# Performance work log

Measured on AMD Instinct MI355X. Metric: run time of the kernel, lower is better.

Reference implementation:

```python
import jax, jax.numpy as jnp
import numpy as np

SIZE = 416
STRIDES = (8, 16, 32)
A = 3            # anchors per scale
C = 20           # num classes
CONF_THRESH = 0.001
NMS_THRESH = 0.5
ANCHORS = [[1.0,1.5],[2.0,3.0],[3.0,2.5],[1.5,3.5],[3.0,4.0],[4.0,3.0],[3.5,5.0],[5.0,4.5],[8.0,8.0]]


def _make_grids():
    # Mirrors myYOLOv3.init_grid, including the off-by-one that leaves the
    # LAST cell of each scale with zero anchor_wh (slice start:index).
    anchors = np.asarray(ANCHORS, np.float32).reshape(3, 3, 2)
    anchors = anchors * np.array([4.0, 2.0, 1.0], np.float32).reshape(3, 1, 1)
    grids, awhs, strs = [], [], []
    for i, s in enumerate(STRIDES):
        ws, hs = SIZE // s, SIZE // s
        ys, xs = np.meshgrid(np.arange(hs), np.arange(ws), indexing='ij')
        g = np.stack([xs, ys], -1).reshape(hs * ws, 1, 2).astype(np.float32)
        grids.append(np.broadcast_to(g, (hs * ws, A, 2)))
        awh = np.broadcast_to(anchors[i], (hs * ws, A, 2)).copy()
        awh[hs * ws - 1] = 0.0  # replicate init_grid bug
        awhs.append(awh)
        strs.append(np.full((hs * ws, A), s, np.float32))
    grid = jnp.asarray(np.concatenate(grids, 0))      # [HWt, A, 2]
    awh = jnp.asarray(np.concatenate(awhs, 0))        # [HWt, A, 2]
    stride = jnp.asarray(np.concatenate(strs, 0).reshape(-1))  # [HWt*A]
    return grid, awh, stride


def _flatten(pred):
    # [B, A*(1+C+4), H, W] -> obj [B, HW*A], cls [B, HW*A, C], xywh [B, HW, A, 4]
    B, abC, H, W = pred.shape
    p = jnp.transpose(pred, (0, 2, 3, 1)).reshape(B, H * W, abC)
    obj = p[..., :A].reshape(B, H * W * A)
    cls = p[..., A:A * (1 + C)].reshape(B, H * W * A, C)
    xywh = p[..., A * (1 + C):].reshape(B, H * W, A, 4)
    return obj, cls, xywh


def _nms(boxes, scores, cls_inds, valid):
    # Greedy per-class NMS: processing in global score order and suppressing
    # only same-class overlaps is exactly equivalent to the per-class loops
    # in myYOLOv3.postprocess.
    N = boxes.shape[0]
    order = jnp.argsort(-scores)
    b = boxes[order]
    c = cls_inds[order]
    v = valid[order]
    areas = (b[:, 2] - b[:, 0]) * (b[:, 3] - b[:, 1])
    idx = jnp.arange(N)

    def body(i, carry):
        keep, supp = carry
        ki = v[i] & ~supp[i]
        xx1 = jnp.maximum(b[i, 0], b[:, 0])
        yy1 = jnp.maximum(b[i, 1], b[:, 1])
        xx2 = jnp.minimum(b[i, 2], b[:, 2])
        yy2 = jnp.minimum(b[i, 3], b[:, 3])
        inter = jnp.maximum(1e-28, xx2 - xx1) * jnp.maximum(1e-28, yy2 - yy1)
        iou = inter / (areas[i] + areas - inter)
        supp = supp | (ki & (iou > NMS_THRESH) & (c == c[i]) & (idx > i))
        return keep.at[i].set(ki), supp

    keep_s, _ = jax.lax.fori_loop(
        0, N, body, (jnp.zeros(N, bool), jnp.zeros(N, bool)))
    return jnp.zeros(N, bool).at[order].set(keep_s)


def setup_inputs() -> dict:
    key = jax.random.key(0)
    k1, k2, k3 = jax.random.split(key, 3)
    B, abC = 64, A * (1 + 4 + C)
    return {
        'pred_1': jax.random.normal(k1, (B, abC, 52, 52), jnp.float32),
        'pred_2': jax.random.normal(k2, (B, abC, 26, 26), jnp.float32),
        'pred_3': jax.random.normal(k3, (B, abC, 13, 13), jnp.float32),
    }


def reference(pred_1, pred_2, pred_3):
    grid, awh, stride = _make_grids()
    objs, clss, xys = zip(*[_flatten(p) for p in (pred_1, pred_2, pred_3)])
    obj = jnp.concatenate(objs, 1)    # [B, N]
    cls = jnp.concatenate(clss, 1)    # [B, N, C]
    xywh = jnp.concatenate(xys, 1)    # [B, HWt, A, 4]
    B = obj.shape[0]

    # decode_boxes: sigmoid/exp + grid add + stride scale -> xyxy pixels
    cxy = jax.nn.sigmoid(xywh[..., :2]) + grid
    bwh = jnp.exp(xywh[..., 2:]) * awh
    bbox = jnp.concatenate([cxy, bwh], -1).reshape(B, -1, 4)  # [B, N, 4]
    half = bbox[..., 2:] * 0.5
    st = stride[None, :, None]
    boxes = jnp.concatenate([(bbox[..., :2] - half) * st,
                             (bbox[..., :2] + half) * st], -1)  # [B,N,4]

    all_obj = jax.nn.sigmoid(obj[0])                 # [N]
    all_bbox = boxes[0] / SIZE                       # normalized
    all_class = jax.nn.softmax(cls[0], axis=1) * all_obj[:, None]
    cls_inds = jnp.argmax(all_class, axis=1)
    scores = jnp.max(all_class, axis=1)
    valid = scores >= CONF_THRESH

    keep = _nms(all_bbox, scores, cls_inds, valid)

    # bboxes *= scale; clip to [0, SIZE-1]; /= scale
    bboxes = jnp.clip(all_bbox * SIZE, 0.0, SIZE - 1.0) / SIZE
    return bboxes, scores, cls_inds, keep
```

## Files before the change

### kernel.cpp

```cpp
#include <hip/hip_runtime.h>
#include <stdint.h>

typedef unsigned long long u64;
typedef unsigned int u32;

#define NA 10647
#define NCLS 20
#define CAPB 1024
#define CAP2 640
#define NWP 11
#define OUT_SCORES 42588
#define OUT_CLS    53235
#define OUT_KEEP   63882

__constant__ float c_aw[9] = {4.f,8.f,12.f, 3.f,6.f,8.f, 3.5f,5.f,8.f};
__constant__ float c_ah[9] = {6.f,12.f,10.f, 7.f,8.f,6.f, 5.f,4.5f,8.f};

__device__ __forceinline__ float sig(float x){ return 1.0f/(1.0f+expf(-x)); }

__device__ __forceinline__ u64 shflxor64(u64 v, int m){
    int lo = __shfl_xor((int)(u32)(v & 0xffffffffull), m);
    int hi = __shfl_xor((int)(u32)(v >> 32), m);
    return ((u64)(u32)hi << 32) | (u32)lo;
}

__global__ void decode_kernel(const float* __restrict__ p1, const float* __restrict__ p2,
                              const float* __restrict__ p3, float* __restrict__ out,
                              float4* __restrict__ box4, u64* __restrict__ bucket,
                              int* __restrict__ cls_cnt, float* __restrict__ keep_out)
{
    int n = blockIdx.x*128 + threadIdx.x;
    if (n >= NA) return;
    const float* p; int base, W, HW, L; float s;
    if (n < 8112)      { p=p1; base=0;     W=52; HW=2704; s=8.f;  L=0; }
    else if (n<10140)  { p=p2; base=8112;  W=26; HW=676;  s=16.f; L=1; }
    else               { p=p3; base=10140; W=13; HW=169;  s=32.f; L=2; }
    int r  = n - base;
    int hw = r/3, a = r - hw*3;
    int h  = hw/W, w = hw - h*W;

    float obj = sig(p[(size_t)a*HW + hw]);

    float e[NCLS];
    #pragma unroll
    for (int c=0;c<NCLS;c++) e[c] = p[(size_t)(3 + a*NCLS + c)*HW + hw];
    float xmax = e[0];
    #pragma unroll
    for (int c=1;c<NCLS;c++) xmax = fmaxf(xmax, e[c]);
    float ssum = 0.f;
    #pragma unroll
    for (int c=0;c<NCLS;c++){ e[c] = expf(e[c]-xmax); ssum += e[c]; }
    float best = -1.0f; int bi = 0;
    #pragma unroll
    for (int c=0;c<NCLS;c++){ float v = (e[c]/ssum)*obj; if (v > best){ best=v; bi=c; } }

    int xb = 63 + a*4;
    float tx = p[(size_t)(xb+0)*HW + hw];
    float ty = p[(size_t)(xb+1)*HW + hw];
    float tw = p[(size_t)(xb+2)*HW + hw];
    float th = p[(size_t)(xb+3)*HW + hw];
    float aw = c_aw[L*3+a], ah = c_ah[L*3+a];
    if (hw == HW-1){ aw=0.f; ah=0.f; }
    float cx = sig(tx) + (float)w;
    float cy = sig(ty) + (float)h;
    float bw = expf(tw)*aw, bh = expf(th)*ah;
    float hx = bw*0.5f,  hy = bh*0.5f;
    float x1 = ((cx-hx)*s)/416.0f;
    float y1 = ((cy-hy)*s)/416.0f;
    float x2 = ((cx+hx)*s)/416.0f;
    float y2 = ((cy+hy)*s)/416.0f;

    out[n*4+0] = fminf(fmaxf(x1*416.0f,0.f),415.f)/416.0f;
    out[n*4+1] = fminf(fmaxf(y1*416.0f,0.f),415.f)/416.0f;
    out[n*4+2] = fminf(fmaxf(x2*416.0f,0.f),415.f)/416.0f;
    out[n*4+3] = fminf(fmaxf(y2*416.0f,0.f),415.f)/416.0f;
    out[OUT_SCORES + n] = best;
    out[OUT_CLS    + n] = (float)bi;

    box4[n] = make_float4(x1,y1,x2,y2);

    u64 key = ((u64)(~__float_as_uint(best)) << 32) | (u32)n;
    int pos = atomicAdd(&cls_cnt[bi], 1);
    if (pos < CAPB) bucket[(size_t)bi*CAPB + pos] = key;
    else keep_out[n] = 0.0f;
}

__global__ __launch_bounds__(1024) void sort_kernel(
    const u64* __restrict__ bucket, const int* __restrict__ cls_cnt,
    const float4* __restrict__ box4, u64* __restrict__ skeys_g,
    float4* __restrict__ sbox_g)
{
    __shared__ u64 ex[CAPB];
    int b = blockIdx.x, t = threadIdx.x;
    int cnt = cls_cnt[b];
    int Mall = (cnt < CAPB) ? cnt : CAPB;
    u64 v = (t < Mall) ? bucket[(size_t)b*CAPB + t] : ~0ull;

    #pragma unroll
    for (int k = 2; k <= CAPB; k <<= 1){
        bool asc = ((t & k) == 0);
        for (int j = k >> 1; j >= 64; j >>= 1){
            ex[t] = v;
            __syncthreads();
            u64 w = ex[t ^ j];
            bool takeMin = (((t & j) == 0) == asc);
            v = takeMin ? (v < w ? v : w) : (v > w ? v : w);
            __syncthreads();
        }
        int j0 = (k >> 1 > 32) ? 32 : (k >> 1);
        #pragma unroll
        for (int j = j0; j >= 1; j >>= 1){
            u64 w = shflxor64(v, j);
            bool takeMin = (((t & j) == 0) == asc);
            v = takeMin ? (v < w ? v : w) : (v > w ? v : w);
        }
    }

    skeys_g[(size_t)b*CAPB + t] = v;
    if (t < CAP2){
        int M = (cnt < CAP2) ? cnt : CAP2;
        float4 bx = make_float4(0.f,0.f,0.f,0.f);
        if (t < M) bx = box4[(u32)v];
        sbox_g[(size_t)b*CAP2 + t] = bx;
    }
}

__global__ __launch_bounds__(256) void build_kernel(
    const float4* __restrict__ sbox_g, const int* __restrict__ cls_cnt,
    u64* __restrict__ maskg)
{
    __shared__ float4 cb_s[CAP2];
    __shared__ float  ca_s[CAP2];
    int rc = blockIdx.x, b = blockIdx.y;
    int tid = threadIdx.x, wv = tid>>6, ln = tid&63;
    int cnt = cls_cnt[b];
    int M  = (cnt < CAP2) ? cnt : CAP2;
    int MC = (M + 63) & ~63;
    if (rc*64 >= MC) return;
    for (int t = tid; t < CAP2; t += 256){
        float4 bx = sbox_g[(size_t)b*CAP2 + t];
        cb_s[t] = bx;
        ca_s[t] = (bx.z - bx.x) * (bx.w - bx.y);
    }
    __syncthreads();
    int nw = MC >> 6;
    for (int ri = wv; ri < 64; ri += 4){
        int rrow = rc*64 + ri;
        float4 rb = cb_s[rrow]; float ra = ca_s[rrow];
        for (int w = rc; w < nw; w++){
            int j = w*64 + ln;
            float4 cb = cb_s[j]; float ca = ca_s[j];
            float xx1=fmaxf(rb.x,cb.x), yy1=fmaxf(rb.y,cb.y);
            float xx2=fminf(rb.z,cb.z), yy2=fminf(rb.w,cb.w);
            float inter=fmaxf(1e-28f,xx2-xx1)*fmaxf(1e-28f,yy2-yy1);
            float iou = inter/((ra+ca)-inter);
            u64 bm = __ballot(iou > 0.5f);
            if (ln == 0) maskg[((size_t)b*CAP2 + rrow)*NWP + w] = bm;
        }
    }
}

__global__ __launch_bounds__(512) void scan_kernel(
    const u64* __restrict__ maskg, const u64* __restrict__ skeys_g,
    const int* __restrict__ cls_cnt, float* __restrict__ keep_out)
{
    __shared__ u64 lm[CAP2*NWP];
    __shared__ u64 validw_s[CAP2/64], remw[CAP2/64], keepw_s[CAP2/64];
    __shared__ u64 keep_bc;
    int b = blockIdx.x, tid = threadIdx.x, wv = tid>>6, ln = tid&63;
    int cnt = cls_cnt[b];
    int Mall = (cnt < CAPB) ? cnt : CAPB;
    int M    = (cnt < CAP2) ? cnt : CAP2;
    int MC = (M + 63) & ~63;
    int nw = MC >> 6;

    for (int t = tid; t < MC*NWP; t += 512) lm[t] = maskg[(size_t)b*CAP2*NWP + t];
    for (int w0 = wv; w0 < nw; w0 += 8){
        int t = w0*64 + ln;
        u64 key = skeys_g[(size_t)b*CAPB + t];
        float sc = __uint_as_float(~(u32)(key >> 32));
        u64 bm = __ballot(t < M && sc >= 0.001f);
        if (ln == 0) validw_s[w0] = bm;
    }
    for (int w = tid; w < nw; w += 512) remw[w] = 0ull;
    __syncthreads();

    for (int c = 0; c < nw; c++){
        if (wv == 0){
            u64 W = lm[(c*64 + ln)*NWP + c];
            u64 rem  = remw[c];
            u64 cand = validw_s[c] & ~rem;
            u64 keepw = 0;
            while (cand){
                int bp  = __builtin_ctzll(cand);
                int bps = __builtin_amdgcn_readfirstlane(bp);
                u64 rowm = ((u64)(u32)__builtin_amdgcn_readlane((int)(u32)(W>>32), bps) << 32)
                         |        (u32)__builtin_amdgcn_readlane((int)(u32)(W),     bps);
                keepw |= 1ull << bps;
                cand  &= ~(rowm | (1ull << bps));
            }
            if (ln == 0){ keepw_s[c] = keepw; keep_bc = keepw; }
        }
        __syncthreads();
        u64 kk = keep_bc;
        if (kk && c + 1 < nw){
            int i0 = tid >> 4;
            int wsl = tid & 15;
            int w = c + 1 + wsl;
            u64 acc = 0;
            if (w < nw){
                if ((kk >> i0) & 1ull)        acc  = lm[(c*64 + i0)*NWP + w];
                int i1 = i0 + 32;
                if ((kk >> i1) & 1ull)        acc |= lm[(c*64 + i1)*NWP + w];
            }
            acc |= shflxor64(acc, 16);
            acc |= shflxor64(acc, 32);
            if (ln < 16 && w < nw && acc) atomicOr(&remw[w], acc);
        }
        __syncthreads();
    }

    for (int t = tid; t < Mall; t += 512){
        u32 o = (u32)skeys_g[(size_t)b*CAPB + t];
        float kv = 0.0f;
        if (t < M) kv = ((keepw_s[t>>6] >> (t&63)) & 1ull) ? 1.0f : 0.0f;
        keep_out[o] = kv;
    }
}

extern "C" void kernel_launch(void* const* d_in, const int* in_sizes, int n_in,
                              void* d_out, int out_size, void* d_ws, size_t ws_size,
                              hipStream_t stream) {
    const float* p1 = (const float*)d_in[0];
    const float* p2 = (const float*)d_in[1];
    const float* p3 = (const float*)d_in[2];
    float* out = (float*)d_out;

    char* ws = (char*)d_ws;
    size_t off = 0;
    auto alloc = [&](size_t bytes)->void*{ void* p = ws + off; off += (bytes + 255) & ~(size_t)255; return p; };
    float4* box4    = (float4*)alloc((size_t)NA*16);
    u64*    bucket  = (u64*)   alloc((size_t)NCLS*CAPB*8);
    int*    cls_cnt = (int*)   alloc((size_t)NCLS*4);
    u64*    skeys_g = (u64*)   alloc((size_t)NCLS*CAPB*8);
    float4* sbox_g  = (float4*)alloc((size_t)NCLS*CAP2*16);
    u64*    maskg   = (u64*)   alloc((size_t)NCLS*CAP2*NWP*8);

    hipMemsetAsync(cls_cnt, 0, NCLS*sizeof(int), stream);
    decode_kernel<<<(NA+127)/128, 128, 0, stream>>>(p1,p2,p3,out,box4,bucket,cls_cnt,
                                                    out + OUT_KEEP);
    sort_kernel <<<NCLS, 1024, 0, stream>>>(bucket, cls_cnt, box4, skeys_g, sbox_g);
    build_kernel<<<dim3(CAP2/64, NCLS), 256, 0, stream>>>(sbox_g, cls_cnt, maskg);
    scan_kernel <<<NCLS, 512, 0, stream>>>(maskg, skeys_g, cls_cnt, out + OUT_KEEP);
}
```

Before: 181.6 us.

## Fuse per-class bucketing, sort, IoU mask build and NMS scan into one kernel

Decode now writes a packed class|score|index key per anchor, with no global atomics or memset. A single 1024-thread block per class then gathers its members through a shared-memory atomic counter, bitonic-sorts them, builds the IoU bitmask in LDS and runs the greedy scan. This removes three kernel launches, a memset and the global round-trips for the sorted keys, boxes and mask. In exchange, every block scans all ~10.6k keys, the IoU mask build now runs on only 20 blocks instead of up to 200, and LDS use per block is higher.

```diff
diff --git a/kernel.cpp b/kernel.cpp
--- a/kernel.cpp
+++ b/kernel.cpp
@@ -8,7 +8,7 @@
 #define NCLS 20
 #define CAPB 1024
 #define CAP2 640
-#define NWP 11
+#define NWP 10
 #define OUT_SCORES 42588
 #define OUT_CLS    53235
 #define OUT_KEEP   63882
@@ -26,8 +26,7 @@
 
 __global__ void decode_kernel(const float* __restrict__ p1, const float* __restrict__ p2,
                               const float* __restrict__ p3, float* __restrict__ out,
-                              float4* __restrict__ box4, u64* __restrict__ bucket,
-                              int* __restrict__ cls_cnt, float* __restrict__ keep_out)
+                              float4* __restrict__ box4, u64* __restrict__ ckey)
 {
     int n = blockIdx.x*128 + threadIdx.x;
     if (n >= NA) return;
@@ -79,31 +78,48 @@
 
     box4[n] = make_float4(x1,y1,x2,y2);
 
-    u64 key = ((u64)(~__float_as_uint(best)) << 32) | (u32)n;
-    int pos = atomicAdd(&cls_cnt[bi], 1);
-    if (pos < CAPB) bucket[(size_t)bi*CAPB + pos] = key;
-    else keep_out[n] = 0.0f;
-}
-
-__global__ __launch_bounds__(1024) void sort_kernel(
-    const u64* __restrict__ bucket, const int* __restrict__ cls_cnt,
-    const float4* __restrict__ box4, u64* __restrict__ skeys_g,
-    float4* __restrict__ sbox_g)
+    ckey[n] = ((u64)(u32)bi << 46) | ((u64)(~__float_as_uint(best)) << 14) | (u64)(u32)n;
+}
+
+__global__ __launch_bounds__(1024) void nms_kernel(
+    const u64* __restrict__ ckey, const float4* __restrict__ box4,
+    u32* __restrict__ sidx_g, float* __restrict__ keep_out)
 {
-    __shared__ u64 ex[CAPB];
-    int b = blockIdx.x, t = threadIdx.x;
-    int cnt = cls_cnt[b];
+    __shared__ u64   lm[CAP2*NWP];
+    __shared__ float4 sbox[CAP2];
+    __shared__ float  sarea[CAP2];
+    __shared__ u64 validw_s[CAP2/64], remw[CAP2/64], keepw_s[CAP2/64];
+    __shared__ u64 keep_bc;
+    __shared__ int cnt_s;
+    int b = blockIdx.x, tid = threadIdx.x, wv = tid>>6, ln = tid&63;
+
+    if (tid == 0) cnt_s = 0;
+    __syncthreads();
+
+    for (int n = tid; n < NA; n += 1024){
+        u64 ck = ckey[n];
+        if ((int)(ck >> 46) == b){
+            int pos = atomicAdd(&cnt_s, 1);
+            if (pos < CAPB) lm[pos] = ck & ((1ull<<46)-1ull);
+            else keep_out[n] = 0.0f;
+        }
+    }
+    __syncthreads();
+    int cnt  = cnt_s;
     int Mall = (cnt < CAPB) ? cnt : CAPB;
-    u64 v = (t < Mall) ? bucket[(size_t)b*CAPB + t] : ~0ull;
-
+    int M    = (cnt < CAP2) ? cnt : CAP2;
+    int MC   = (M + 63) & ~63;
+    int nw   = MC >> 6;
+
+    u64 v = (tid < Mall) ? lm[tid] : ~0ull;
     #pragma unroll
     for (int k = 2; k <= CAPB; k <<= 1){
-        bool asc = ((t & k) == 0);
+        bool asc = ((tid & k) == 0);
         for (int j = k >> 1; j >= 64; j >>= 1){
-            ex[t] = v;
+            lm[tid] = v;
             __syncthreads();
-            u64 w = ex[t ^ j];
-            bool takeMin = (((t & j) == 0) == asc);
+            u64 w = lm[tid ^ j];
+            bool takeMin = (((tid & j) == 0) == asc);
             v = takeMin ? (v < w ? v : w) : (v > w ? v : w);
             __syncthreads();
         }
@@ -111,78 +127,41 @@
         #pragma unroll
         for (int j = j0; j >= 1; j >>= 1){
             u64 w = shflxor64(v, j);
-            bool takeMin = (((t & j) == 0) == asc);
+            bool takeMin = (((tid & j) == 0) == asc);
             v = takeMin ? (v < w ? v : w) : (v > w ? v : w);
         }
     }
 
-    skeys_g[(size_t)b*CAPB + t] = v;
-    if (t < CAP2){
-        int M = (cnt < CAP2) ? cnt : CAP2;
+    u32 idx = (u32)(v & 0x3FFFull);
+    sidx_g[(size_t)b*CAPB + tid] = idx;
+    {
+        float sc = __uint_as_float(~(u32)(v >> 14));
+        u64 bm = __ballot(tid < M && sc >= 0.001f);
+        if (ln == 0 && wv < nw) validw_s[wv] = bm;
+    }
+    if (tid < CAP2){
         float4 bx = make_float4(0.f,0.f,0.f,0.f);
-        if (t < M) bx = box4[(u32)v];
-        sbox_g[(size_t)b*CAP2 + t] = bx;
-    }
-}
-
-__global__ __launch_bounds__(256) void build_kernel(
-    const float4* __restrict__ sbox_g, const int* __restrict__ cls_cnt,
-    u64* __restrict__ maskg)
-{
-    __shared__ float4 cb_s[CAP2];
-    __shared__ float  ca_s[CAP2];
-    int rc = blockIdx.x, b = blockIdx.y;
-    int tid = threadIdx.x, wv = tid>>6, ln = tid&63;
-    int cnt = cls_cnt[b];
-    int M  = (cnt < CAP2) ? cnt : CAP2;
-    int MC = (M + 63) & ~63;
-    if (rc*64 >= MC) return;
-    for (int t = tid; t < CAP2; t += 256){
-        float4 bx = sbox_g[(size_t)b*CAP2 + t];
-        cb_s[t] = bx;
-        ca_s[t] = (bx.z - bx.x) * (bx.w - bx.y);
-    }
-    __syncthreads();
-    int nw = MC >> 6;
-    for (int ri = wv; ri < 64; ri += 4){
-        int rrow = rc*64 + ri;
-        float4 rb = cb_s[rrow]; float ra = ca_s[rrow];
+        if (tid < M) bx = box4[idx];
+        sbox[tid]  = bx;
+        sarea[tid] = (bx.z - bx.x) * (bx.w - bx.y);
+    }
+    if (tid < CAP2/64) remw[tid] = 0ull;
+    __syncthreads();
+
+    for (int r = wv; r < MC; r += 16){
+        int rc = r >> 6;
+        float4 rb = sbox[r]; float ra = sarea[r];
         for (int w = rc; w < nw; w++){
             int j = w*64 + ln;
-            float4 cb = cb_s[j]; float ca = ca_s[j];
+            float4 cb = sbox[j]; float ca = sarea[j];
             float xx1=fmaxf(rb.x,cb.x), yy1=fmaxf(rb.y,cb.y);
             float xx2=fminf(rb.z,cb.z), yy2=fminf(rb.w,cb.w);
             float inter=fmaxf(1e-28f,xx2-xx1)*fmaxf(1e-28f,yy2-yy1);
             float iou = inter/((ra+ca)-inter);
             u64 bm = __ballot(iou > 0.5f);
-            if (ln == 0) maskg[((size_t)b*CAP2 + rrow)*NWP + w] = bm;
-        }
-    }
-}
-
-__global__ __launch_bounds__(512) void scan_kernel(
-    const u64* __restrict__ maskg, const u64* __restrict__ skeys_g,
-    const int* __restrict__ cls_cnt, float* __restrict__ keep_out)
-{
-    __shared__ u64 lm[CAP2*NWP];
-    __shared__ u64 validw_s[CAP2/64], remw[CAP2/64], keepw_s[CAP2/64];
-    __shared__ u64 keep_bc;
-    int b = blockIdx.x, tid = threadIdx.x, wv = tid>>6, ln = tid&63;
-    int cnt = cls_cnt[b];
-    int Mall = (cnt < CAPB) ? cnt : CAPB;
-    int M    = (cnt < CAP2) ? cnt : CAP2;
-    int MC = (M + 63) & ~63;
-    int nw = MC >> 6;
-
-    for (int t = tid; t < MC*NWP; t += 512) lm[t] = maskg[(size_t)b*CAP2*NWP + t];
-    for (int w0 = wv; w0 < nw; w0 += 8){
-        int t = w0*64 + ln;
-        u64 key = skeys_g[(size_t)b*CAPB + t];
-        float sc = __uint_as_float(~(u32)(key >> 32));
-        u64 bm = __ballot(t < M && sc >= 0.001f);
-        if (ln == 0) validw_s[w0] = bm;
-    }
-    for (int w = tid; w < nw; w += 512) remw[w] = 0ull;
+            if (ln == 0) lm[r*NWP + w] = bm;
+        }
+    }
     __syncthreads();
 
     for (int c = 0; c < nw; c++){
@@ -204,15 +183,11 @@
         __syncthreads();
         u64 kk = keep_bc;
         if (kk && c + 1 < nw){
-            int i0 = tid >> 4;
+            int i0  = tid >> 4;
             int wsl = tid & 15;
             int w = c + 1 + wsl;
             u64 acc = 0;
-            if (w < nw){
-                if ((kk >> i0) & 1ull)        acc  = lm[(c*64 + i0)*NWP + w];
-                int i1 = i0 + 32;
-                if ((kk >> i1) & 1ull)        acc |= lm[(c*64 + i1)*NWP + w];
-            }
+            if (w < nw && ((kk >> i0) & 1ull)) acc = lm[(c*64 + i0)*NWP + w];
             acc |= shflxor64(acc, 16);
             acc |= shflxor64(acc, 32);
             if (ln < 16 && w < nw && acc) atomicOr(&remw[w], acc);
@@ -220,8 +195,8 @@
         __syncthreads();
     }
 
-    for (int t = tid; t < Mall; t += 512){
-        u32 o = (u32)skeys_g[(size_t)b*CAPB + t];
+    for (int t = tid; t < Mall; t += 1024){
+        u32 o = sidx_g[(size_t)b*CAPB + t];
         float kv = 0.0f;
         if (t < M) kv = ((keepw_s[t>>6] >> (t&63)) & 1ull) ? 1.0f : 0.0f;
         keep_out[o] = kv;
@@ -239,17 +214,10 @@
     char* ws = (char*)d_ws;
     size_t off = 0;
     auto alloc = [&](size_t bytes)->void*{ void* p = ws + off; off += (bytes + 255) & ~(size_t)255; return p; };
-    float4* box4    = (float4*)alloc((size_t)NA*16);
-    u64*    bucket  = (u64*)   alloc((size_t)NCLS*CAPB*8);
-    int*    cls_cnt = (int*)   alloc((size_t)NCLS*4);
-    u64*    skeys_g = (u64*)   alloc((size_t)NCLS*CAPB*8);
-    float4* sbox_g  = (float4*)alloc((size_t)NCLS*CAP2*16);
-    u64*    maskg   = (u64*)   alloc((size_t)NCLS*CAP2*NWP*8);
-
-    hipMemsetAsync(cls_cnt, 0, NCLS*sizeof(int), stream);
-    decode_kernel<<<(NA+127)/128, 128, 0, stream>>>(p1,p2,p3,out,box4,bucket,cls_cnt,
-                                                    out + OUT_KEEP);
-    sort_kernel <<<NCLS, 1024, 0, stream>>>(bucket, cls_cnt, box4, skeys_g, sbox_g);
-    build_kernel<<<dim3(CAP2/64, NCLS), 256, 0, stream>>>(sbox_g, cls_cnt, maskg);
-    scan_kernel <<<NCLS, 512, 0, stream>>>(maskg, skeys_g, cls_cnt, out + OUT_KEEP);
-}
+    float4* box4 = (float4*)alloc((size_t)NA*16);
+    u64*    ckey = (u64*)   alloc((size_t)NA*8);
+    u32*    sidx = (u32*)   alloc((size_t)NCLS*CAPB*4);
+
+    decode_kernel<<<(NA+127)/128, 128, 0, stream>>>(p1,p2,p3,out,box4,ckey);
+    nms_kernel  <<<NCLS, 1024, 0, stream>>>(ckey, box4, sidx, out + OUT_KEEP);
+}
```

Measured after the change: 181.7 us. No clear change (+0.0%).
